# Kernel optimization log

Hardware: AMD Instinct MI355X
Metric: run time of the kernel (lower is better)

## Reference

```python
import jax, jax.numpy as jnp
import numpy as np

B, T, C = 4, 2048, 1024
H = 16
D = C // H  # head_dim = 64
SCALE = D ** -0.5


def setup_inputs() -> dict:
    key = jax.random.key(0)
    ks = jax.random.split(key, 5)
    x = jax.random.normal(ks[0], (B, T, C), dtype=jnp.float32)
    w_qkv = jax.random.normal(ks[1], (3 * C, C), dtype=jnp.float32) * (C ** -0.5)
    b_qkv = jnp.zeros((3 * C,), dtype=jnp.float32)
    w_proj = jax.random.normal(ks[2], (C, C), dtype=jnp.float32) * (C ** -0.5)
    b_proj = jnp.zeros((C,), dtype=jnp.float32)
    return {"x": x, "w_qkv": w_qkv, "b_qkv": b_qkv, "w_proj": w_proj, "b_proj": b_proj}


def reference(x, w_qkv, b_qkv, w_proj, b_proj):
    b, t, c = x.shape
    # fused qkv projection (torch Linear: x @ W.T + b)
    qkv = x @ w_qkv.T + b_qkv                      # [B, T, 3C]
    q, k, v = jnp.split(qkv, 3, axis=2)
    # [B, T, C] -> [B, H, T, D]
    q = q.reshape(b, t, H, D).transpose(0, 2, 1, 3)
    k = k.reshape(b, t, H, D).transpose(0, 2, 1, 3)
    v = v.reshape(b, t, H, D).transpose(0, 2, 1, 3)
    att = jnp.einsum('bhqd,bhkd->bhqk', q, k) * SCALE
    causal = jnp.tril(jnp.ones((t, t), dtype=bool))  # True = keep
    att = jnp.where(causal, att, -jnp.inf)
    att = jax.nn.softmax(att, axis=-1)
    out = jnp.einsum('bhqk,bhkd->bhqd', att, v)
    out = out.transpose(0, 2, 1, 3).reshape(b, t, c)
    return out @ w_proj.T + b_proj
```

## Files before the change

kernel.cpp:

```cpp
#include <hip/hip_runtime.h>

typedef unsigned short u16;
typedef __attribute__((ext_vector_type(8))) short short8;
typedef __attribute__((ext_vector_type(4))) float f32x4;
typedef __attribute__((ext_vector_type(16))) float f32x16;
typedef __attribute__((ext_vector_type(2))) unsigned uint2v;
typedef __attribute__((ext_vector_type(4))) unsigned u32x4;

#define AS1 __attribute__((address_space(1)))
#define AS3 __attribute__((address_space(3)))

constexpr int Bn = 4, Tn = 2048, Cn = 1024, Hn = 16, Dn = 64;
constexpr float SCL_LOG2E = 0.125f * 1.44269504088896f;

__device__ __forceinline__ u16 f2bf(float f) {
  union { float f; unsigned u; } v; v.f = f;
  unsigned r = v.u + 0x7FFFu + ((v.u >> 16) & 1u);
  return (u16)(r >> 16);
}

__device__ __forceinline__ unsigned cvtpk_bf16(float a, float b) {
  unsigned r;
  asm("v_cvt_pk_bf16_f32 %0, %1, %2" : "=v"(r) : "v"(a), "v"(b));
  return r;
}

__global__ void cast_f32_to_bf16(const float* __restrict__ in, u16* __restrict__ out, int n4) {
  int i = blockIdx.x * 256 + threadIdx.x;
  if (i >= n4) return;
  float4 v = ((const float4*)in)[i];
  ushort4 o;
  o.x = f2bf(v.x); o.y = f2bf(v.y); o.z = f2bf(v.z); o.w = f2bf(v.w);
  ((ushort4*)out)[i] = o;
}

__device__ __forceinline__ void store_out(u16* p, float v) { *p = f2bf(v); }
__device__ __forceinline__ void store_out(float* p, float v) { *p = v; }

template <int BM, int BN, typename OT>
__global__ __launch_bounds__(512) void gemm8(
    const u16* __restrict__ A, const u16* __restrict__ Bm,
    const float* __restrict__ bias, OT* __restrict__ C,
    int M, int N, int K, int nbn, int qcols, float qscale)
{
  constexpr int NHA = BM / 128, NHB = BN / 128, NH = NHA + NHB;
  constexpr int MR = BM / 32;
  constexpr int NR = BN / 64;
  __shared__ u16 As[2][BM * 64];
  __shared__ u16 Bs[2][BN * 64];

  const int tid = threadIdx.x;
  const int lane = tid & 63;
  const int w = tid >> 6;
  const int wm = w >> 2, wn = w & 3;
  const int l15 = lane & 15, lg = lane >> 4;

  const int nwg = gridDim.x;
  const int wg = (blockIdx.x & 7) * (nwg >> 3) + (blockIdx.x >> 3);
  const int m0 = (wg / nbn) * BM;
  const int n0 = (wg % nbn) * BN;
  const int NT = K >> 6;

  const int wrow = wm * (BM / 2);
  const int wcol = wn * (BN / 4);

  f32x4 acc[MR][NR] = {};

  auto stage_half = [&](int tt, int h) {
    if (tt >= NT) return;
    const int bu = tt & 1;
#pragma unroll
    for (int it = 0; it < 2; ++it) {
      const int c = it * 512 + tid;
      const int row = c >> 3;
      const int cs = (c & 7) ^ (row & 7);
      if (h < NHA) {
        const u16* g = A + (size_t)(m0 + h * 128 + row) * K + tt * 64 + cs * 8;
        __builtin_amdgcn_global_load_lds((const AS1 void*)g,
            (AS3 void*)(&As[bu][(h * 128 + row) * 64 + (c & 7) * 8]), 16, 0, 0);
      } else {
        const int rb = (h - NHA) * 128 + row;
        const u16* g = Bm + (size_t)(n0 + rb) * K + tt * 64 + cs * 8;
        __builtin_amdgcn_global_load_lds((const AS1 void*)g,
            (AS3 void*)(&Bs[bu][rb * 64 + (c & 7) * 8]), 16, 0, 0);
      }
    }
  };

  auto readA = [&](int bu, int mh, short8 (*a)[2]) {
#pragma unroll
    for (int i = 0; i < MR / 2; ++i)
#pragma unroll
      for (int ks = 0; ks < 2; ++ks) {
        const int ra = wrow + (mh * (MR / 2) + i) * 16 + l15;
        a[i][ks] = *(const short8*)(&As[bu][ra * 64 + (((ks * 4 + lg) ^ (ra & 7)) << 3)]);
      }
  };
  auto readB = [&](int bu, int nh, short8 (*b)[2]) {
#pragma unroll
    for (int j = 0; j < NR / 2; ++j)
#pragma unroll
      for (int ks = 0; ks < 2; ++ks) {
        const int rb = wcol + (nh * (NR / 2) + j) * 16 + l15;
        b[j][ks] = *(const short8*)(&Bs[bu][rb * 64 + (((ks * 4 + lg) ^ (rb & 7)) << 3)]);
      }
  };
  auto mmaq = [&](int mh, int nh, short8 (*a)[2], short8 (*b)[2]) {
    __builtin_amdgcn_s_setprio(1);
#pragma unroll
    for (int i = 0; i < MR / 2; ++i)
#pragma unroll
      for (int j = 0; j < NR / 2; ++j)
#pragma unroll
        for (int ks = 0; ks < 2; ++ks)
          acc[mh * (MR / 2) + i][nh * (NR / 2) + j] =
              __builtin_amdgcn_mfma_f32_16x16x32_bf16(
                  a[i][ks], b[j][ks], acc[mh * (MR / 2) + i][nh * (NR / 2) + j], 0, 0, 0);
    __builtin_amdgcn_s_setprio(0);
  };

#pragma unroll
  for (int h = 0; h < NH; ++h) stage_half(0, h);
  stage_half(1, 0);
  asm volatile("s_waitcnt vmcnt(2)" ::: "memory");
  __builtin_amdgcn_sched_barrier(0);
  __builtin_amdgcn_s_barrier();

  for (int t = 0; t < NT; ++t) {
    const int bu = t & 1;
    short8 a0[MR / 2][2], a1[MR / 2][2], b0[NR / 2][2], b1[NR / 2][2];
    readA(bu, 0, a0);
    readB(bu, 0, b0);
    stage_half(t + 1, 1);
    __builtin_amdgcn_s_barrier();
    mmaq(0, 0, a0, b0);
    __builtin_amdgcn_s_barrier();
    readB(bu, 1, b1);
    stage_half(t + 1, 2);
    __builtin_amdgcn_s_barrier();
    mmaq(0, 1, a0, b1);
    __builtin_amdgcn_s_barrier();
    readA(bu, 1, a1);
    if constexpr (NH > 3) stage_half(t + 1, 3);
    __builtin_amdgcn_s_barrier();
    mmaq(1, 1, a1, b1);
    __builtin_amdgcn_s_barrier();
    stage_half(t + 2, 0);
    __builtin_amdgcn_s_barrier();
    mmaq(1, 0, a1, b0);
    if (t + 2 < NT) {
      asm volatile("s_waitcnt vmcnt(2)" ::: "memory");
      __builtin_amdgcn_sched_barrier(0);
    } else if (t < NT - 1) {
      asm volatile("s_waitcnt vmcnt(0)" ::: "memory");
      __builtin_amdgcn_sched_barrier(0);
    }
    __builtin_amdgcn_s_barrier();
  }

#pragma unroll
  for (int i = 0; i < MR; ++i) {
    const int rowg = m0 + wrow + i * 16 + lg * 4;
#pragma unroll
    for (int j = 0; j < NR; ++j) {
      const int colg = n0 + wcol + j * 16 + l15;
      const float sc = (colg < qcols) ? qscale : 1.0f;
      const float bv = bias[colg];
#pragma unroll
      for (int r = 0; r < 4; ++r)
        store_out(C + (size_t)(rowg + r) * N + colg, (acc[i][j][r] + bv) * sc);
    }
  }
}

__global__ __launch_bounds__(256) void transpose_v(
    const u16* __restrict__ qkv, u16* __restrict__ vt)
{
  __shared__ u16 tile[64][72];
  const int bh = blockIdx.x >> 5;
  const int tt = blockIdx.x & 31;
  const int b = bh >> 4;
  const int h = bh & 15;
  const int tid = threadIdx.x;
  const int trow = tid >> 2;
  const int dseg = tid & 3;

  const u16* src = qkv + (size_t)(b * Tn + tt * 64 + trow) * (3 * Cn) + 2 * Cn + h * Dn + dseg * 16;
  short8 v0 = *(const short8*)src;
  short8 v1 = *(const short8*)(src + 8);
#pragma unroll
  for (int e = 0; e < 8; ++e) {
    tile[dseg * 16 + e][trow] = (u16)v0[e];
    tile[dseg * 16 + 8 + e][trow] = (u16)v1[e];
  }
  __syncthreads();

  const int drow = tid >> 2;
  const int tseg = tid & 3;
  u16* dst = vt + (size_t)(bh * Dn + drow) * Tn + tt * 64 + tseg * 16;
  *(short8*)dst = *(const short8*)&tile[drow][tseg * 16];
  *(short8*)(dst + 8) = *(const short8*)&tile[drow][tseg * 16 + 8];
}

__global__ __launch_bounds__(256) void attn_kernel(
    const u16* __restrict__ qkv, const u16* __restrict__ vt, u16* __restrict__ att)
{
  __shared__ u16 Ks[2][64 * 64];
  __shared__ u16 Vs[2][64 * 64];
  const int tid = threadIdx.x;
  const int lane = tid & 63;
  const int w = tid >> 6;
  const int l31 = lane & 31;
  const int hi = lane >> 5;

  const int blk = blockIdx.x;
  const int qt = (Tn / 128 - 1) - (blk >> 6);
  const int bh = blk & 63;
  const int b = bh >> 4;
  const int h = bh & 15;
  const int q0w = qt * 128 + w * 32;
  const int rowbase = b * Tn;
  const int koff = Cn + h * Dn;
  const size_t vbase = (size_t)bh * Dn * Tn;
  const int nt = 2 * qt + 2;
  const int ntw = 2 * qt + 1 + (w >> 1);

  short8 qf[4];
  {
    const u16* qp = qkv + (size_t)(rowbase + q0w + l31) * (3 * Cn) + h * Dn + hi * 8;
#pragma unroll
    for (int sub = 0; sub < 4; ++sub) qf[sub] = *(const short8*)(qp + sub * 16);
  }

  float m_r = -1e30f, l_r = 0.f;
  f32x16 oacc[2] = {};

#define STAGE(buf, t_)                                                            \
  {                                                                               \
    const int kt_ = (t_) * 64;                                                    \
    _Pragma("unroll")                                                             \
    for (int it = 0; it < 2; ++it) {                                              \
      int c = it * 256 + tid;                                                     \
      int row = c >> 3;                                                           \
      int cs = (c & 7) ^ (row & 7);                                               \
      const u16* gk = qkv + (size_t)(rowbase + kt_ + row) * (3 * Cn) + koff + cs * 8; \
      __builtin_amdgcn_global_load_lds((const AS1 void*)gk, (AS3 void*)(&Ks[buf][c * 8]), 16, 0, 0); \
      const u16* gv = vt + vbase + (size_t)row * Tn + kt_ + cs * 8;               \
      __builtin_amdgcn_global_load_lds((const AS1 void*)gv, (AS3 void*)(&Vs[buf][c * 8]), 16, 0, 0); \
    }                                                                             \
  }

  STAGE(0, 0);
  __syncthreads();

  for (int t = 0; t < nt; ++t) {
    const int cur = t & 1;
    if (t + 1 < nt) STAGE(cur ^ 1, t + 1);
    if (t < ntw) {
      const int kt = t * 64;
      const u16* Kb = Ks[cur];
      const u16* Vb = Vs[cur];

      f32x16 s0 = {}, s1 = {};
#pragma unroll
      for (int sub = 0; sub < 4; ++sub) {
        const int ch = sub * 2 + hi;
        const int r0 = l31;
        short8 kf0 = *(const short8*)(Kb + r0 * 64 + ((ch ^ (r0 & 7)) << 3));
        s0 = __builtin_amdgcn_mfma_f32_32x32x16_bf16(kf0, qf[sub], s0, 0, 0, 0);
        const int r1 = 32 + l31;
        short8 kf1 = *(const short8*)(Kb + r1 * 64 + ((ch ^ (r1 & 7)) << 3));
        s1 = __builtin_amdgcn_mfma_f32_32x32x16_bf16(kf1, qf[sub], s1, 0, 0, 0);
      }

      if (kt + 63 > q0w) {
        const int qa = q0w + l31;
#pragma unroll
        for (int r = 0; r < 16; ++r) {
          const int k0 = kt + ((r & 3) + 8 * (r >> 2)) + 4 * hi;
          if (k0 > qa) s0[r] = -1e30f;
          if (k0 + 32 > qa) s1[r] = -1e30f;
        }
      }

      float mx = s0[0];
#pragma unroll
      for (int r = 1; r < 16; ++r) mx = fmaxf(mx, s0[r]);
#pragma unroll
      for (int r = 0; r < 16; ++r) mx = fmaxf(mx, s1[r]);
      mx = fmaxf(mx, __shfl_xor(mx, 32));

      if (__any(mx > m_r + 8.f)) {
        const float mnew = fmaxf(m_r, mx);
        const float a = __builtin_amdgcn_exp2f(m_r - mnew);
        m_r = mnew;
        l_r *= a;
#pragma unroll
        for (int r = 0; r < 16; ++r) { oacc[0][r] *= a; oacc[1][r] *= a; }
      }

      float ps = 0.f;
#pragma unroll
      for (int r = 0; r < 16; ++r) {
        s0[r] = __builtin_amdgcn_exp2f(s0[r] - m_r); ps += s0[r];
        s1[r] = __builtin_amdgcn_exp2f(s1[r] - m_r); ps += s1[r];
      }
      ps += __shfl_xor(ps, 32);
      l_r += ps;

      short8 pfr[4];
#pragma unroll
      for (int ks = 0; ks < 4; ++ks) {
        const f32x16& sv = (ks < 2) ? s0 : s1;
        const int base = (ks & 1) * 8;
        unsigned a0 = cvtpk_bf16(sv[base + 0], sv[base + 1]);
        unsigned a1 = cvtpk_bf16(sv[base + 2], sv[base + 3]);
        unsigned b0 = cvtpk_bf16(sv[base + 4], sv[base + 5]);
        unsigned b1 = cvtpk_bf16(sv[base + 6], sv[base + 7]);
        uint2v s_0 = __builtin_amdgcn_permlane32_swap(a0, b0, false, false);
        uint2v s_1 = __builtin_amdgcn_permlane32_swap(a1, b1, false, false);
        union { u32x4 u; short8 s; } cvt;
        cvt.u = (u32x4){s_0.x, s_1.x, s_0.y, s_1.y};
        pfr[ks] = cvt.s;
      }

#pragma unroll
      for (int j = 0; j < 2; ++j) {
        const int rv = j * 32 + l31;
        const int rsw = (rv & 7) << 3;
#pragma unroll
        for (int ks = 0; ks < 4; ++ks) {
          short8 vf = *(const short8*)(Vb + rv * 64 + (((ks * 2 + hi) << 3) ^ rsw));
          oacc[j] = __builtin_amdgcn_mfma_f32_32x32x16_bf16(vf, pfr[ks], oacc[j], 0, 0, 0);
        }
      }
    }
    __syncthreads();
  }

  {
    const float inv = __builtin_amdgcn_rcpf(l_r);
    u16* orow = att + (size_t)(rowbase + q0w + l31) * Cn + h * Dn + hi * 4;
#pragma unroll
    for (int j = 0; j < 2; ++j)
#pragma unroll
      for (int g = 0; g < 4; ++g) {
        ushort4 o;
#pragma unroll
        for (int c = 0; c < 4; ++c) o[c] = f2bf(oacc[j][g * 4 + c] * inv);
        *(ushort4*)(orow + j * 32 + g * 8) = o;
      }
  }
#undef STAGE
}

extern "C" void kernel_launch(void* const* d_in, const int* in_sizes, int n_in,
                              void* d_out, int out_size, void* d_ws, size_t ws_size,
                              hipStream_t stream) {
  const float* x      = (const float*)d_in[0];
  const float* w_qkv  = (const float*)d_in[1];
  const float* b_qkv  = (const float*)d_in[2];
  const float* w_proj = (const float*)d_in[3];
  const float* b_proj = (const float*)d_in[4];
  float* out = (float*)d_out;

  char* ws = (char*)d_ws;
  u16* x_bf     = (u16*)(ws);
  u16* wqkv_bf  = (u16*)(ws + 16777216);
  u16* wproj_bf = (u16*)(ws + 16777216 + 6291456);
  u16* qkv      = (u16*)(ws + 25165824);
  u16* att      = (u16*)(ws + 75497472);
  u16* vt       = x_bf;

  const int M = Bn * Tn;

  cast_f32_to_bf16<<<(M * Cn / 4 + 255) / 256, 256, 0, stream>>>(x, x_bf, M * Cn / 4);
  cast_f32_to_bf16<<<(3 * Cn * Cn / 4 + 255) / 256, 256, 0, stream>>>(w_qkv, wqkv_bf, 3 * Cn * Cn / 4);
  cast_f32_to_bf16<<<(Cn * Cn / 4 + 255) / 256, 256, 0, stream>>>(w_proj, wproj_bf, Cn * Cn / 4);

  gemm8<128, 256, u16><<<768, 512, 0, stream>>>(
      x_bf, wqkv_bf, b_qkv, qkv, M, 3 * Cn, Cn, 12, Cn, SCL_LOG2E);

  transpose_v<<<Bn * Hn * (Tn / 64), 256, 0, stream>>>(qkv, vt);

  attn_kernel<<<Bn * Hn * (Tn / 128), 256, 0, stream>>>(qkv, vt, att);

  gemm8<128, 256, float><<<256, 512, 0, stream>>>(
      att, wproj_bf, b_proj, out, M, Cn, Cn, 4, 0, 1.0f);
}
```

Baseline: 182.1 us.

## Interleave B tile halves by wave column so each half feeds one MFMA phase

Specializes the GEMM to 128x256 tiles and restages the B operand so LDS buffer half h holds, for every wave, the 32 columns consumed in MFMA phase nh=h. A and B staging are separated, and the vmcnt waits are reordered so the second B half of the next tile can still be in flight while the first phases compute. This aims to hide global-to-LDS latency better, at the cost of more complex wait accounting and risk of premature reads if the counts are off.

```diff
diff --git a/kernel.cpp b/kernel.cpp
--- a/kernel.cpp
+++ b/kernel.cpp
@@ -37,17 +37,14 @@
 __device__ __forceinline__ void store_out(u16* p, float v) { *p = f2bf(v); }
 __device__ __forceinline__ void store_out(float* p, float v) { *p = v; }
 
-template <int BM, int BN, typename OT>
+template <typename OT>
 __global__ __launch_bounds__(512) void gemm8(
     const u16* __restrict__ A, const u16* __restrict__ Bm,
     const float* __restrict__ bias, OT* __restrict__ C,
     int M, int N, int K, int nbn, int qcols, float qscale)
 {
-  constexpr int NHA = BM / 128, NHB = BN / 128, NH = NHA + NHB;
-  constexpr int MR = BM / 32;
-  constexpr int NR = BN / 64;
-  __shared__ u16 As[2][BM * 64];
-  __shared__ u16 Bs[2][BN * 64];
+  __shared__ u16 As[2][128 * 64];
+  __shared__ u16 Bs[2][2][128 * 64];
 
   const int tid = threadIdx.x;
   const int lane = tid & 63;
@@ -57,16 +54,15 @@
 
   const int nwg = gridDim.x;
   const int wg = (blockIdx.x & 7) * (nwg >> 3) + (blockIdx.x >> 3);
-  const int m0 = (wg / nbn) * BM;
-  const int n0 = (wg % nbn) * BN;
+  const int m0 = (wg / nbn) * 128;
+  const int n0 = (wg % nbn) * 256;
   const int NT = K >> 6;
 
-  const int wrow = wm * (BM / 2);
-  const int wcol = wn * (BN / 4);
-
-  f32x4 acc[MR][NR] = {};
-
-  auto stage_half = [&](int tt, int h) {
+  const int wrow = wm * 64;
+
+  f32x4 acc[4][4] = {};
+
+  auto stage_A = [&](int tt) {
     if (tt >= NT) return;
     const int bu = tt & 1;
 #pragma unroll
@@ -74,96 +70,105 @@
       const int c = it * 512 + tid;
       const int row = c >> 3;
       const int cs = (c & 7) ^ (row & 7);
-      if (h < NHA) {
-        const u16* g = A + (size_t)(m0 + h * 128 + row) * K + tt * 64 + cs * 8;
-        __builtin_amdgcn_global_load_lds((const AS1 void*)g,
-            (AS3 void*)(&As[bu][(h * 128 + row) * 64 + (c & 7) * 8]), 16, 0, 0);
-      } else {
-        const int rb = (h - NHA) * 128 + row;
-        const u16* g = Bm + (size_t)(n0 + rb) * K + tt * 64 + cs * 8;
-        __builtin_amdgcn_global_load_lds((const AS1 void*)g,
-            (AS3 void*)(&Bs[bu][rb * 64 + (c & 7) * 8]), 16, 0, 0);
-      }
+      const u16* g = A + (size_t)(m0 + row) * K + tt * 64 + cs * 8;
+      __builtin_amdgcn_global_load_lds((const AS1 void*)g,
+          (AS3 void*)(&As[bu][c * 8]), 16, 0, 0);
+    }
+  };
+  auto stage_B = [&](int tt, int h) {
+    if (tt >= NT) return;
+    const int bu = tt & 1;
+#pragma unroll
+    for (int it = 0; it < 2; ++it) {
+      const int c = it * 512 + tid;
+      const int i = c >> 3;
+      const int cs = (c & 7) ^ (i & 7);
+      const int grow = n0 + ((i >> 5) << 6) + (h << 5) + (i & 31);
+      const u16* g = Bm + (size_t)grow * K + tt * 64 + cs * 8;
+      __builtin_amdgcn_global_load_lds((const AS1 void*)g,
+          (AS3 void*)(&Bs[bu][h][c * 8]), 16, 0, 0);
     }
   };
 
   auto readA = [&](int bu, int mh, short8 (*a)[2]) {
 #pragma unroll
-    for (int i = 0; i < MR / 2; ++i)
+    for (int i = 0; i < 2; ++i)
 #pragma unroll
       for (int ks = 0; ks < 2; ++ks) {
-        const int ra = wrow + (mh * (MR / 2) + i) * 16 + l15;
+        const int ra = wrow + (mh * 2 + i) * 16 + l15;
         a[i][ks] = *(const short8*)(&As[bu][ra * 64 + (((ks * 4 + lg) ^ (ra & 7)) << 3)]);
       }
   };
   auto readB = [&](int bu, int nh, short8 (*b)[2]) {
 #pragma unroll
-    for (int j = 0; j < NR / 2; ++j)
+    for (int j = 0; j < 2; ++j)
 #pragma unroll
       for (int ks = 0; ks < 2; ++ks) {
-        const int rb = wcol + (nh * (NR / 2) + j) * 16 + l15;
-        b[j][ks] = *(const short8*)(&Bs[bu][rb * 64 + (((ks * 4 + lg) ^ (rb & 7)) << 3)]);
+        const int i = wn * 32 + j * 16 + l15;
+        b[j][ks] = *(const short8*)(&Bs[bu][nh][i * 64 + (((ks * 4 + lg) ^ (i & 7)) << 3)]);
       }
   };
   auto mmaq = [&](int mh, int nh, short8 (*a)[2], short8 (*b)[2]) {
     __builtin_amdgcn_s_setprio(1);
 #pragma unroll
-    for (int i = 0; i < MR / 2; ++i)
-#pragma unroll
-      for (int j = 0; j < NR / 2; ++j)
+    for (int i = 0; i < 2; ++i)
+#pragma unroll
+      for (int j = 0; j < 2; ++j)
 #pragma unroll
         for (int ks = 0; ks < 2; ++ks)
-          acc[mh * (MR / 2) + i][nh * (NR / 2) + j] =
-              __builtin_amdgcn_mfma_f32_16x16x32_bf16(
-                  a[i][ks], b[j][ks], acc[mh * (MR / 2) + i][nh * (NR / 2) + j], 0, 0, 0);
+          acc[mh * 2 + i][nh * 2 + j] = __builtin_amdgcn_mfma_f32_16x16x32_bf16(
+              a[i][ks], b[j][ks], acc[mh * 2 + i][nh * 2 + j], 0, 0, 0);
     __builtin_amdgcn_s_setprio(0);
   };
 
-#pragma unroll
-  for (int h = 0; h < NH; ++h) stage_half(0, h);
-  stage_half(1, 0);
-  asm volatile("s_waitcnt vmcnt(2)" ::: "memory");
+  stage_A(0);
+  stage_B(0, 0);
+  stage_B(0, 1);
+  stage_A(1);
+  asm volatile("s_waitcnt vmcnt(4)" ::: "memory");
   __builtin_amdgcn_sched_barrier(0);
   __builtin_amdgcn_s_barrier();
 
   for (int t = 0; t < NT; ++t) {
     const int bu = t & 1;
-    short8 a0[MR / 2][2], a1[MR / 2][2], b0[NR / 2][2], b1[NR / 2][2];
+    short8 a0[2][2], a1[2][2], b0[2][2], b1[2][2];
     readA(bu, 0, a0);
     readB(bu, 0, b0);
-    stage_half(t + 1, 1);
+    stage_B(t + 1, 0);
     __builtin_amdgcn_s_barrier();
     mmaq(0, 0, a0, b0);
+    if (t + 1 < NT) asm volatile("s_waitcnt vmcnt(4)" ::: "memory");
+    else            asm volatile("s_waitcnt vmcnt(0)" ::: "memory");
+    __builtin_amdgcn_sched_barrier(0);
     __builtin_amdgcn_s_barrier();
     readB(bu, 1, b1);
-    stage_half(t + 1, 2);
+    stage_B(t + 1, 1);
     __builtin_amdgcn_s_barrier();
     mmaq(0, 1, a0, b1);
     __builtin_amdgcn_s_barrier();
     readA(bu, 1, a1);
-    if constexpr (NH > 3) stage_half(t + 1, 3);
     __builtin_amdgcn_s_barrier();
     mmaq(1, 1, a1, b1);
     __builtin_amdgcn_s_barrier();
-    stage_half(t + 2, 0);
+    stage_A(t + 2);
     __builtin_amdgcn_s_barrier();
     mmaq(1, 0, a1, b0);
     if (t + 2 < NT) {
+      asm volatile("s_waitcnt vmcnt(4)" ::: "memory");
+      __builtin_amdgcn_sched_barrier(0);
+    } else if (t + 1 < NT) {
       asm volatile("s_waitcnt vmcnt(2)" ::: "memory");
       __builtin_amdgcn_sched_barrier(0);
-    } else if (t < NT - 1) {
-      asm volatile("s_waitcnt vmcnt(0)" ::: "memory");
-      __builtin_amdgcn_sched_barrier(0);
-    }
-    __builtin_amdgcn_s_barrier();
-  }
-
-#pragma unroll
-  for (int i = 0; i < MR; ++i) {
+    }
+    __builtin_amdgcn_s_barrier();
+  }
+
+#pragma unroll
+  for (int i = 0; i < 4; ++i) {
     const int rowg = m0 + wrow + i * 16 + lg * 4;
 #pragma unroll
-    for (int j = 0; j < NR; ++j) {
-      const int colg = n0 + wcol + j * 16 + l15;
+    for (int j = 0; j < 4; ++j) {
+      const int colg = n0 + wn * 64 + j * 16 + l15;
       const float sc = (colg < qcols) ? qscale : 1.0f;
       const float bv = bias[colg];
 #pragma unroll
@@ -378,13 +383,13 @@
   cast_f32_to_bf16<<<(3 * Cn * Cn / 4 + 255) / 256, 256, 0, stream>>>(w_qkv, wqkv_bf, 3 * Cn * Cn / 4);
   cast_f32_to_bf16<<<(Cn * Cn / 4 + 255) / 256, 256, 0, stream>>>(w_proj, wproj_bf, Cn * Cn / 4);
 
-  gemm8<128, 256, u16><<<768, 512, 0, stream>>>(
+  gemm8<u16><<<768, 512, 0, stream>>>(
       x_bf, wqkv_bf, b_qkv, qkv, M, 3 * Cn, Cn, 12, Cn, SCL_LOG2E);
 
   transpose_v<<<Bn * Hn * (Tn / 64), 256, 0, stream>>>(qkv, vt);
 
   attn_kernel<<<Bn * Hn * (Tn / 128), 256, 0, stream>>>(qkv, vt, att);
 
-  gemm8<128, 256, float><<<256, 512, 0, stream>>>(
+  gemm8<float><<<256, 512, 0, stream>>>(
       att, wproj_bf, b_proj, out, M, Cn, Cn, 4, 0, 1.0f);
 }
```

New measurement: 176.5 us. -3.1%, faster.
